# Performance work log

Measured on AMD Instinct MI355X. Metric: run time of the kernel, lower is better.

Reference implementation:

```python
import jax, jax.numpy as jnp
import numpy as np

N = 2048; C_IN = 2; H = 32; EMB = 16; OUT = 1; HORIZON = 12
B = 32; T = 16

def setup_inputs() -> dict:
    key = jax.random.key(0)
    ks = jax.random.split(key, 10)
    s = 0.05
    return {
        "x":  jax.random.normal(ks[0], (B, T, N, C_IN), dtype=jnp.float32),
        "E1": jax.random.normal(ks[1], (N, EMB), dtype=jnp.float32) * 0.1,
        "E2": jax.random.normal(ks[2], (N, EMB), dtype=jnp.float32) * 0.1,
        "Wx": jax.random.normal(ks[3], (C_IN, 4 * H), dtype=jnp.float32) * s,
        "bx": jnp.zeros((4 * H,), dtype=jnp.float32),
        "Wh": jax.random.normal(ks[4], (H, 4 * H), dtype=jnp.float32) * s,
        "bh": jnp.zeros((4 * H,), dtype=jnp.float32),
        "Wp": jax.random.normal(ks[5], (H, OUT * HORIZON), dtype=jnp.float32) * s,
        "bp": jnp.zeros((OUT * HORIZON,), dtype=jnp.float32),
    }

def reference(x, E1, E2, Wx, bx, Wh, bh, Wp, bp):
    Bb, Tt, Nn, _ = x.shape
    # adaptive adjacency: softmax(relu(E1 @ E2^T)) over last dim  [N,N]
    A = jax.nn.softmax(jax.nn.relu(E1 @ E2.T), axis=-1)

    def step(carry, xt):
        h, c = carry  # [B,N,H]
        # fused graph-conv gates: (A @ xt) Wx + (A @ h) Wh + biases -> [B,N,4H]
        gates = (jnp.einsum('ij,bjc->bic', A, xt) @ Wx + bx
                 + jnp.einsum('ij,bjh->bih', A, h) @ Wh + bh)
        i, f, o, g = jnp.split(gates, 4, axis=-1)
        i = jax.nn.sigmoid(i); f = jax.nn.sigmoid(f); o = jax.nn.sigmoid(o)
        g = jnp.tanh(g)
        c_t = f * c + i * g
        h_t = o * jnp.tanh(c_t)
        return (h_t, c_t), None

    h0 = jnp.zeros((Bb, Nn, H), dtype=x.dtype)
    c0 = jnp.zeros((Bb, Nn, H), dtype=x.dtype)
    (h_last, _), _ = jax.lax.scan(step, (h0, c0), jnp.transpose(x, (1, 0, 2, 3)))
    out = h_last @ Wp + bp                      # [B,N,horizon*out]
    out = out.reshape(Bb, Nn, HORIZON, OUT)
    return jnp.transpose(out, (0, 2, 1, 3))     # [B,horizon,N,out]
```

## Files before the change

### kernel.cpp

```cpp
#include <hip/hip_runtime.h>
#include <hip/hip_bf16.h>
#include <cstddef>
#include <cstdint>

#define NN 2048
#define CIN 2
#define HH 32
#define EMB 16
#define HOR 12
#define BB 32
#define TT 16
#define GC 128
#define XCOLS 1024
#define HCOLS 1024

#define ATILE_STRIDE 65536
#define BTILE_STRIDE 32768
#define LOPLANE 2097152

typedef __attribute__((ext_vector_type(8))) _Float16 f16x8;
typedef __attribute__((ext_vector_type(16))) float f32x16;

__device__ __forceinline__ void load_lds16(const void* g, void* l) {
    __builtin_amdgcn_global_load_lds(
        (const __attribute__((address_space(1))) void*)g,
        (__attribute__((address_space(3))) void*)l, 16, 0, 0);
}

__global__ __launch_bounds__(256) void precompute(const float* __restrict__ E1,
                                                  const float* __restrict__ E2,
                                                  const float* __restrict__ x,
                                                  const float* __restrict__ Wx,
                                                  const float* __restrict__ bx,
                                                  const float* __restrict__ Wh,
                                                  const float* __restrict__ bh,
                                                  _Float16* __restrict__ A2,
                                                  _Float16* __restrict__ B2x,
                                                  _Float16* __restrict__ W16,
                                                  float* __restrict__ Wxr,
                                                  float* __restrict__ bfold) {
    const int blk = blockIdx.x;
    const int tid = threadIdx.x;

    if (blk < NN) {
        const int i = blk;
        __shared__ float red[256];
        float e1[EMB];
#pragma unroll
        for (int k = 0; k < EMB; ++k) e1[k] = E1[i * EMB + k];

        float s[8];
        float mx = -1e30f;
#pragma unroll
        for (int q = 0; q < 8; ++q) {
            const int j = tid * 8 + q;
            float d = 0.f;
#pragma unroll
            for (int k = 0; k < EMB; ++k) d += e1[k] * E2[j * EMB + k];
            d = fmaxf(d, 0.0f);
            s[q] = d;
            mx = fmaxf(mx, d);
        }
        red[tid] = mx;
        __syncthreads();
        for (int off = 128; off > 0; off >>= 1) {
            if (tid < off) red[tid] = fmaxf(red[tid], red[tid + off]);
            __syncthreads();
        }
        mx = red[0];
        __syncthreads();

        float sum = 0.f;
#pragma unroll
        for (int q = 0; q < 8; ++q) { s[q] = expf(s[q] - mx); sum += s[q]; }
        red[tid] = sum;
        __syncthreads();
        for (int off = 128; off > 0; off >>= 1) {
            if (tid < off) red[tid] += red[tid + off];
            __syncthreads();
        }
        const float inv = 1.0f / red[0];
        f16x8 v;
#pragma unroll
        for (int q = 0; q < 8; ++q) v[q] = (_Float16)(s[q] * inv);
        *(f16x8*)(A2 + ((size_t)tid * 2048 + i) * 8) = v;
    } else if (blk < NN + 1024) {
        const int idx = (blk - NN) * 256 + tid;
        const int col = idx & 1023;
        const int jc  = idx >> 10;
        const int bt  = col >> 1;
        const int c   = col & 1;
        const float* xp = x + ((size_t)bt * NN + jc * 8) * CIN + c;
        f16x8 vh, vl;
#pragma unroll
        for (int e = 0; e < 8; ++e) {
            const float v = xp[e * CIN];
            const _Float16 hi = (_Float16)v;
            vh[e] = hi;
            vl[e] = (_Float16)(v - (float)hi);
        }
        const size_t base = ((size_t)jc * 1024 + col) * 8;
        *(f16x8*)(B2x + base) = vh;
        *(f16x8*)(B2x + base + LOPLANE) = vl;
    } else {
#pragma unroll
        for (int r = 0; r < 32; ++r) {
            const int idx = r * 256 + tid;
            const int e  = idx & 7;
            const int ln = (idx >> 3) & 63;
            const int gq = (idx >> 9) & 3;
            const int kh = (idx >> 11) & 1;
            const int k  = kh * 16 + (ln >> 5) * 8 + e;
            const int ch = gq * 32 + (ln & 31);
            const float v = Wh[k * GC + (ch & 3) * HH + (ch >> 2)];
            const _Float16 hi = (_Float16)v;
            W16[idx] = hi;
            W16[8192 + idx] = (_Float16)(v - (float)hi);
        }
        {
            const int idx = tid;
            const int c = idx >> 7, rem = idx & 127;
            const int h = rem >> 2, g = rem & 3;
            Wxr[idx] = Wx[c * GC + g * HH + h];
        }
        if (tid < 128) {
            const int h = tid >> 2, g = tid & 3;
            bfold[tid] = bx[g * HH + h] + bh[g * HH + h];
        }
    }
}

template <int NPROD, int GATE>
__global__ __launch_bounds__(512, 2) void gemm_fused(const _Float16* __restrict__ A2,
                                                     const _Float16* __restrict__ B2,
                                                     float* __restrict__ Cout,
                                                     const float* __restrict__ AX,
                                                     const _Float16* __restrict__ W16,
                                                     const float* __restrict__ Wxr,
                                                     const float* __restrict__ bfold,
                                                     float* __restrict__ cst,
                                                     float* __restrict__ h32,
                                                     _Float16* __restrict__ hTout,
                                                     int t, int last) {
    constexpr int SUBS   = (NPROD == 1) ? 2 : 1;
    constexpr int NT     = 64 / SUBS;
    constexpr int SUBBUF = 4096 + NPROD * 8192;
    constexpr int BUF    = SUBS * SUBBUF;
    constexpr int NBUF   = (NPROD == 1) ? 4 : 6;
    constexpr int PCH    = 256 + NPROD * 512;
    constexpr int NG     = (SUBS * PCH) / 64;
    constexpr int GMAX   = 3;
    constexpr int STAGE_SZ = NBUF * BUF;
    constexpr int SMEMSZ = GATE ? (STAGE_SZ + 1024 + 512 + 2048) : STAGE_SZ;
    __shared__ __align__(16) char smem[SMEMSZ];

    const int tid  = threadIdx.x;
    const int w    = tid >> 6;
    const int lane = tid & 63;

    const int wg = blockIdx.x;
    const int x8 = wg & 7;
    const int s  = wg >> 3;
    const int mb = (x8 >> 1) * 8 + (s & 7);
    const int nb = (x8 & 1) * 4 + (s >> 3);
    const int m0 = mb * 64;
    const int n0 = nb * 128;

    float* wxr_s = nullptr; float* bfl_s = nullptr; float* axs = nullptr;
    if constexpr (GATE) {
        wxr_s = (float*)(smem + STAGE_SZ);
        bfl_s = (float*)(smem + STAGE_SZ + 1024);
        axs   = (float*)(smem + STAGE_SZ + 1536);
        const int b0c = nb * 4;
        if (tid < 64) *(float4*)&wxr_s[tid * 4] = *(const float4*)&Wxr[tid * 4];
        if (tid < 32) *(float4*)&bfl_s[tid * 4] = *(const float4*)&bfold[tid * 4];
        axs[tid] = AX[(size_t)(m0 + (tid & 63)) * XCOLS +
                      ((b0c + (tid >> 7)) * TT + t) * CIN + ((tid >> 6) & 1)];
    }

    const _Float16* gp[GMAX];
    int lbase[GMAX];
    int adv[GMAX];
    bool val[GMAX];
#pragma unroll
    for (int i = 0; i < GMAX; ++i) {
        const int g = w + 8 * i;
        val[i] = (g < NG);
        const int gg = val[i] ? g : 0;
        const int cid  = gg * 64 + lane;
        const int cid0 = gg * 64;
        const int su  = cid / PCH,  r  = cid  - su * PCH;
        const int su0 = cid0 / PCH, r0 = cid0 - su0 * PCH;
        if (r < 256) {
            gp[i]  = A2 + ((size_t)((su * 4 + (r >> 6)) * 2048) + m0 + (r & 63)) * 8;
            adv[i] = SUBS * ATILE_STRIDE;
        } else {
            const int r2 = r - 256;
            gp[i]  = B2 + (size_t)(r2 >> 9) * LOPLANE
                        + ((size_t)((su * 4 + ((r2 & 511) >> 7)) * 1024) + n0 + (r2 & 127)) * 8;
            adv[i] = SUBS * BTILE_STRIDE;
        }
        lbase[i] = su0 * SUBBUF + (r0 < 256 ? r0 * 16 : 4096 + (r0 - 256) * 16);
    }

    const int lrow = lane & 31, lg = lane >> 5;
    const int mi = w >> 2;
    const int gq = w & 3;
    const int wc = gq * 32;
    const int aoff0 = lg * 1024 + (mi * 32 + lrow) * 16;
    const int aoff1 = 2048 + lg * 1024 + (mi * 32 + lrow) * 16;
    const int boff0 = 4096 + lg * 2048 + (wc + lrow) * 16;
    const int boff1 = 4096 + 4096 + lg * 2048 + (wc + lrow) * 16;

    f32x16 acc0 = (f32x16)(0.0f), acc1 = (f32x16)(0.0f);

#define STAGE(BUFI) do {                                                       \
    char* lb = smem + (BUFI) * BUF;                                            \
    _Pragma("unroll")                                                          \
    for (int i = 0; i < GMAX; ++i) if (val[i]) {                               \
        load_lds16(gp[i], lb + lbase[i]);                                      \
        gp[i] += adv[i];                                                       \
    }                                                                          \
} while (0)

#define VMW(NHI, NLO) do {                                                     \
    if (w < 4) asm volatile("s_waitcnt vmcnt(" #NHI ")" ::: "memory");         \
    else       asm volatile("s_waitcnt vmcnt(" #NLO ")" ::: "memory");         \
} while (0)

#define BAR() do {                                                             \
    __builtin_amdgcn_s_barrier();                                              \
    asm volatile("" ::: "memory");                                             \
} while (0)

#define COMPUTE(BUFI) do {                                                     \
    const char* sb = smem + (BUFI) * BUF;                                      \
    _Pragma("unroll")                                                          \
    for (int su = 0; su < SUBS; ++su) {                                        \
        const char* st = sb + su * SUBBUF;                                     \
        f16x8 fa0 = *(const f16x8*)(st + aoff0);                               \
        f16x8 fa1 = *(const f16x8*)(st + aoff1);                               \
        f16x8 fb0 = *(const f16x8*)(st + boff0);                               \
        f16x8 fb1 = *(const f16x8*)(st + boff1);                               \
        acc0 = __builtin_amdgcn_mfma_f32_32x32x16_f16(fa0, fb0, acc0, 0, 0, 0);\
        acc1 = __builtin_amdgcn_mfma_f32_32x32x16_f16(fa1, fb1, acc1, 0, 0, 0);\
        if constexpr (NPROD == 2) {                                            \
            f16x8 fc0 = *(const f16x8*)(st + boff0 + 8192);                    \
            f16x8 fc1 = *(const f16x8*)(st + boff1 + 8192);                    \
            acc0 = __builtin_amdgcn_mfma_f32_32x32x16_f16(fa0, fc0, acc0, 0, 0, 0); \
            acc1 = __builtin_amdgcn_mfma_f32_32x32x16_f16(fa1, fc1, acc1, 0, 0, 0); \
        }                                                                      \
    }                                                                          \
} while (0)

    if constexpr (NPROD == 1) {
        STAGE(0);
        STAGE(1);
#pragma unroll 1
        for (int it = 0; it < NT - 2; ++it) {
            STAGE((it + 2) & 3);
            asm volatile("s_waitcnt vmcnt(6)" ::: "memory");
            BAR();
            COMPUTE(it & 3);
        }
        asm volatile("s_waitcnt vmcnt(3)" ::: "memory");
        BAR();
        COMPUTE((NT - 2) & 3);
        asm volatile("s_waitcnt vmcnt(0)" ::: "memory");
        BAR();
        COMPUTE((NT - 1) & 3);
    } else {
        STAGE(0);
        STAGE(1);
        STAGE(2);
        int bs = 3, bc = 0;
#pragma unroll 1
        for (int it = 0; it < NT - 3; ++it) {
            STAGE(bs);
            VMW(9, 6);
            BAR();
            COMPUTE(bc);
            bs = (bs == 5) ? 0 : bs + 1;
            bc = (bc == 5) ? 0 : bc + 1;
        }
        VMW(6, 4);
        BAR();
        COMPUTE(bc); bc = (bc == 5) ? 0 : bc + 1;
        VMW(3, 2);
        BAR();
        COMPUTE(bc); bc = (bc == 5) ? 0 : bc + 1;
        asm volatile("s_waitcnt vmcnt(0)" ::: "memory");
        BAR();
        COMPUTE(bc);
    }
#undef STAGE
#undef VMW
#undef BAR
#undef COMPUTE

    if constexpr (!GATE) {
        const int colg = n0 + wc + lrow;
#pragma unroll
        for (int r = 0; r < 16; ++r) {
            const int rp = (r & 3) + 8 * (r >> 2) + 4 * lg;
            Cout[(size_t)(m0 + mi * 32 + rp) * XCOLS + colg] = acc0[r] + acc1[r];
        }
    } else {
        f16x8 wbh0 = *(const f16x8*)(W16 + ((size_t)(0 * 4 + gq) * 64 + lane) * 8);
        f16x8 wbh1 = *(const f16x8*)(W16 + ((size_t)(1 * 4 + gq) * 64 + lane) * 8);
        f16x8 wbl0 = *(const f16x8*)(W16 + 8192 + ((size_t)(0 * 4 + gq) * 64 + lane) * 8);
        f16x8 wbl1 = *(const f16x8*)(W16 + 8192 + ((size_t)(1 * 4 + gq) * 64 + lane) * 8);

        _Float16* ahh = (_Float16*)smem;
        _Float16* ahl = (_Float16*)(smem + 17408);
        const int colw = wc + lrow;
#pragma unroll
        for (int r = 0; r < 16; ++r) {
            const int rp = (r & 3) + 8 * (r >> 2) + 4 * lg;
            const float v = acc0[r] + acc1[r];
            const _Float16 hi = (_Float16)v;
            ahh[(mi * 32 + rp) * 136 + colw] = hi;
            ahl[(mi * 32 + rp) * 136 + colw] = (_Float16)(v - (float)hi);
        }
        __syncthreads();

        f32x16 g0 = (f32x16)(0.0f), g1 = (f32x16)(0.0f);
        f32x16 g2 = (f32x16)(0.0f), g3 = (f32x16)(0.0f);
#define GATEB(ACC, b) do {                                                         \
    const int arow = (mi * 32 + lrow) * 136 + (b) * 32 + lg * 8;                   \
    f16x8 fh0 = *(const f16x8*)(ahh + arow);                                       \
    f16x8 fl0 = *(const f16x8*)(ahl + arow);                                       \
    f16x8 fh1 = *(const f16x8*)(ahh + arow + 16);                                  \
    f16x8 fl1 = *(const f16x8*)(ahl + arow + 16);                                  \
    ACC = __builtin_amdgcn_mfma_f32_32x32x16_f16(fh0, wbh0, ACC, 0, 0, 0);         \
    ACC = __builtin_amdgcn_mfma_f32_32x32x16_f16(fh0, wbl0, ACC, 0, 0, 0);         \
    ACC = __builtin_amdgcn_mfma_f32_32x32x16_f16(fl0, wbh0, ACC, 0, 0, 0);         \
    ACC = __builtin_amdgcn_mfma_f32_32x32x16_f16(fh1, wbh1, ACC, 0, 0, 0);         \
    ACC = __builtin_amdgcn_mfma_f32_32x32x16_f16(fh1, wbl1, ACC, 0, 0, 0);         \
    ACC = __builtin_amdgcn_mfma_f32_32x32x16_f16(fl1, wbh1, ACC, 0, 0, 0);         \
} while (0)
        GATEB(g0, 0); GATEB(g1, 1); GATEB(g2, 2); GATEB(g3, 3);
#undef GATEB

        float* gl = (float*)(smem + 34816);
        const int nl2 = tid & 63;
        const int hb  = (tid >> 6) * 4;
        const int b0c = nb * 4;
        const int nd  = m0 + nl2;
        const size_t ntbase = ((size_t)((nd >> 5) * 4 + ((nd >> 3) & 3)) * 1024) * 8 + (nd & 7);

#define POINT(ACC, bi) do {                                                        \
    _Pragma("unroll")                                                              \
    for (int r = 0; r < 16; ++r) {                                                 \
        const int rp = (r & 3) + 8 * (r >> 2) + 4 * lg;                            \
        gl[(mi * 32 + rp) * 132 + gq * 32 + lrow] = ACC[r];                        \
    }                                                                              \
    __syncthreads();                                                               \
    {                                                                              \
        const float ax0 = axs[(bi) * 128 + nl2];                                   \
        const float ax1 = axs[(bi) * 128 + 64 + nl2];                              \
        const int bb = b0c + (bi);                                                 \
        const size_t off = (size_t)nd * HCOLS + bb * HH + hb;                      \
        const float4 co = *(const float4*)(cst + off);                             \
        const float cold[4] = {co.x, co.y, co.z, co.w};                            \
        float cn[4], hn[4];                                                        \
        _Pragma("unroll")                                                          \
        for (int p = 0; p < 4; ++p) {                                              \
            const int hh = hb + p;                                                 \
            const float4 gt = *(const float4*)(gl + nl2 * 132 + hh * 4);           \
            const float a0 = gt.x + bfl_s[hh*4+0] + ax0*wxr_s[hh*4+0] + ax1*wxr_s[128+hh*4+0]; \
            const float a1 = gt.y + bfl_s[hh*4+1] + ax0*wxr_s[hh*4+1] + ax1*wxr_s[128+hh*4+1]; \
            const float a2 = gt.z + bfl_s[hh*4+2] + ax0*wxr_s[hh*4+2] + ax1*wxr_s[128+hh*4+2]; \
            const float a3 = gt.w + bfl_s[hh*4+3] + ax0*wxr_s[hh*4+3] + ax1*wxr_s[128+hh*4+3]; \
            const float i_ = 1.0f / (1.0f + expf(-a0));                            \
            const float f_ = 1.0f / (1.0f + expf(-a1));                            \
            const float o_ = 1.0f / (1.0f + expf(-a2));                            \
            const float g_ = tanhf(a3);                                            \
            const float ct = f_ * cold[p] + i_ * g_;                               \
            cn[p] = ct;                                                            \
            hn[p] = o_ * tanhf(ct);                                                \
        }                                                                          \
        *(float4*)(cst + off) = make_float4(cn[0], cn[1], cn[2], cn[3]);           \
        if (last) *(float4*)(h32 + off) = make_float4(hn[0], hn[1], hn[2], hn[3]); \
        _Pragma("unroll")                                                          \
        for (int p = 0; p < 4; ++p)                                                \
            hTout[ntbase + (size_t)(bb * HH + hb + p) * 8] = (_Float16)hn[p];      \
    }                                                                              \
    __syncthreads();                                                               \
} while (0)
        POINT(g0, 0); POINT(g1, 1); POINT(g2, 2); POINT(g3, 3);
#undef POINT
    }
}

__global__ __launch_bounds__(256) void gate_update(const float* __restrict__ AX,
                                                   const float* __restrict__ Wxr,
                                                   const float* __restrict__ bfold,
                                                   float* __restrict__ c,
                                                   float* __restrict__ h32,
                                                   _Float16* __restrict__ hT) {
    const int n0 = blockIdx.x * 64;
    const int b0 = blockIdx.y * 4;
    const int tid = threadIdx.x;
    __shared__ float wxr[256];
    __shared__ float bfl[128];
    __shared__ float axs[2][64];

    if (tid < 64)  *(float4*)&wxr[tid * 4] = *(const float4*)&Wxr[tid * 4];
    if (tid < 32)  *(float4*)&bfl[tid * 4] = *(const float4*)&bfold[tid * 4];

    const int nl = tid & 63;
    const int hq = tid >> 6;

    const int nd = n0 + nl;
    const size_t ntbase = ((size_t)((nd >> 5) * 4 + ((nd >> 3) & 3)) * 1024) * 8 + (nd & 7);

#pragma unroll 1
    for (int bi = 0; bi < 4; ++bi) {
        const int b = b0 + bi;
        if (bi) __syncthreads();
        if (tid < 128) {
            const int which = tid >> 6, nls = tid & 63;
            axs[which][nls] = AX[(size_t)(n0 + nls) * XCOLS + (b * TT + 0) * CIN + which];
        }
        __syncthreads();

        const float ax0 = axs[0][nl], ax1 = axs[1][nl];
        float cn[8], hn[8];
#pragma unroll
        for (int u = 0; u < 8; ++u) {
            const int h = hq * 8 + u;
            float a0 = bfl[h * 4 + 0] + ax0 * wxr[h * 4 + 0] + ax1 * wxr[128 + h * 4 + 0];
            float a1 = bfl[h * 4 + 1] + ax0 * wxr[h * 4 + 1] + ax1 * wxr[128 + h * 4 + 1];
            float a2 = bfl[h * 4 + 2] + ax0 * wxr[h * 4 + 2] + ax1 * wxr[128 + h * 4 + 2];
            float a3 = bfl[h * 4 + 3] + ax0 * wxr[h * 4 + 3] + ax1 * wxr[128 + h * 4 + 3];
            const float i_ = 1.0f / (1.0f + expf(-a0));
            const float f_ = 1.0f / (1.0f + expf(-a1));
            const float o_ = 1.0f / (1.0f + expf(-a2));
            const float g_ = tanhf(a3);
            const float ct = i_ * g_;
            (void)f_;
            cn[u] = ct;
            hn[u] = o_ * tanhf(ct);
        }
        const size_t off = (size_t)nd * HCOLS + b * HH + hq * 8;
        *(float4*)(c + off)       = make_float4(cn[0], cn[1], cn[2], cn[3]);
        *(float4*)(c + off + 4)   = make_float4(cn[4], cn[5], cn[6], cn[7]);
        *(float4*)(h32 + off)     = make_float4(hn[0], hn[1], hn[2], hn[3]);
        *(float4*)(h32 + off + 4) = make_float4(hn[4], hn[5], hn[6], hn[7]);
#pragma unroll
        for (int u = 0; u < 8; ++u)
            hT[ntbase + (size_t)(b * HH + hq * 8 + u) * 8] = (_Float16)hn[u];
    }
}

__global__ __launch_bounds__(256) void head_kernel(const float* __restrict__ h,
                                                   const float* __restrict__ Wp,
                                                   const float* __restrict__ bp,
                                                   float* __restrict__ out) {
    const int idx = blockIdx.x * 256 + threadIdx.x;
    const int b = idx >> 11;
    const int n = idx & (NN - 1);
    float hv[HH];
    const float* hp = h + (size_t)n * HCOLS + b * HH;
#pragma unroll
    for (int k = 0; k < HH; ++k) hv[k] = hp[k];
#pragma unroll
    for (int th = 0; th < HOR; ++th) {
        float acc = bp[th];
#pragma unroll
        for (int k = 0; k < HH; ++k) acc += hv[k] * Wp[k * HOR + th];
        out[((size_t)b * HOR + th) * NN + n] = acc;
    }
}

extern "C" void kernel_launch(void* const* d_in, const int* in_sizes, int n_in,
                              void* d_out, int out_size, void* d_ws, size_t ws_size,
                              hipStream_t stream) {
    const float* x  = (const float*)d_in[0];
    const float* E1 = (const float*)d_in[1];
    const float* E2 = (const float*)d_in[2];
    const float* Wx = (const float*)d_in[3];
    const float* bx = (const float*)d_in[4];
    const float* Wh = (const float*)d_in[5];
    const float* bh = (const float*)d_in[6];
    const float* Wp = (const float*)d_in[7];
    const float* bp = (const float*)d_in[8];

    char* ws = (char*)d_ws;
    _Float16* A2  = (_Float16*)(ws);
    _Float16* B2x = (_Float16*)(ws + ( 8ull << 20));
    _Float16* hT0 = (_Float16*)(ws + (16ull << 20));
    _Float16* hT1 = (_Float16*)(ws + (20ull << 20));
    float* AX   = (float*)(ws + (24ull << 20));
    float* cst  = (float*)(ws + (32ull << 20));
    float* h32  = (float*)(ws + (40ull << 20));
    float* Wxr  = (float*)(ws + (48ull << 20) + 65536);
    float* bfold= (float*)(ws + (48ull << 20) + 131072);
    _Float16* W16 = (_Float16*)(ws + (48ull << 20) + 262144);
    _Float16* hTb[2] = {hT0, hT1};

    precompute<<<NN + 1024 + 1, 256, 0, stream>>>(E1, E2, x, Wx, bx, Wh, bh,
                                                  A2, B2x, W16, Wxr, bfold);

    gemm_fused<2, 0><<<256, 512, 0, stream>>>(A2, B2x, AX, nullptr, nullptr, nullptr,
                                              nullptr, nullptr, nullptr, nullptr, 0, 0);

    gate_update<<<dim3(NN / 64, BB / 4), 256, 0, stream>>>(AX, Wxr, bfold,
                                                           cst, h32, hTb[0]);
    for (int t = 1; t < TT; ++t) {
        gemm_fused<1, 1><<<256, 512, 0, stream>>>(A2, hTb[(t + 1) & 1], nullptr, AX,
                                                  W16, Wxr, bfold, cst, h32,
                                                  hTb[t & 1], t, t == TT - 1 ? 1 : 0);
    }

    head_kernel<<<(BB * NN) / 256, 256, 0, stream>>>(h32, Wp, bp, (float*)d_out);
}
```

Baseline: 546.0 us.

## Transpose E2 and compute adjacency softmax one row per wavefront with shuffles

Adds a small kernel that transposes E2 so the adjacency-row computation reads it with coalesced loads. Each wavefront now handles a full row of 2048 columns, 32 per lane, and reduces max and sum with wave shuffles instead of block-wide shared-memory reductions and syncthreads. The A2 store becomes scattered 2-byte writes rather than 16-byte vector stores. This adds one extra kernel launch and more register pressure from the 32-element array.

```diff
diff --git a/kernel.cpp b/kernel.cpp
--- a/kernel.cpp
+++ b/kernel.cpp
@@ -27,8 +27,16 @@
         (__attribute__((address_space(3))) void*)l, 16, 0, 0);
 }
 
+__global__ __launch_bounds__(256) void e2_transpose(const float* __restrict__ E2,
+                                                    float* __restrict__ E2T) {
+    const int idx = blockIdx.x * 256 + threadIdx.x;
+    const int k = idx >> 11;
+    const int j = idx & 2047;
+    E2T[idx] = E2[j * EMB + k];
+}
+
 __global__ __launch_bounds__(256) void precompute(const float* __restrict__ E1,
-                                                  const float* __restrict__ E2,
+                                                  const float* __restrict__ E2T,
                                                   const float* __restrict__ x,
                                                   const float* __restrict__ Wx,
                                                   const float* __restrict__ bx,
@@ -42,50 +50,41 @@
     const int blk = blockIdx.x;
     const int tid = threadIdx.x;
 
-    if (blk < NN) {
-        const int i = blk;
-        __shared__ float red[256];
+    if (blk < 512) {
+        const int i = blk * 4 + (tid >> 6);
+        const int l = tid & 63;
         float e1[EMB];
 #pragma unroll
         for (int k = 0; k < EMB; ++k) e1[k] = E1[i * EMB + k];
 
-        float s[8];
-        float mx = -1e30f;
-#pragma unroll
-        for (int q = 0; q < 8; ++q) {
-            const int j = tid * 8 + q;
-            float d = 0.f;
-#pragma unroll
-            for (int k = 0; k < EMB; ++k) d += e1[k] * E2[j * EMB + k];
-            d = fmaxf(d, 0.0f);
-            s[q] = d;
-            mx = fmaxf(mx, d);
-        }
-        red[tid] = mx;
-        __syncthreads();
-        for (int off = 128; off > 0; off >>= 1) {
-            if (tid < off) red[tid] = fmaxf(red[tid], red[tid + off]);
-            __syncthreads();
-        }
-        mx = red[0];
-        __syncthreads();
-
+        float s[32];
+#pragma unroll
+        for (int c = 0; c < 32; ++c) s[c] = 0.f;
+#pragma unroll
+        for (int k = 0; k < EMB; ++k) {
+            const float ek = e1[k];
+            const float* p = E2T + k * 2048 + l;
+#pragma unroll
+            for (int c = 0; c < 32; ++c) s[c] = fmaf(ek, p[c * 64], s[c]);
+        }
+        float mx = 0.f;
+#pragma unroll
+        for (int c = 0; c < 32; ++c) { s[c] = fmaxf(s[c], 0.f); mx = fmaxf(mx, s[c]); }
+#pragma unroll
+        for (int off = 32; off > 0; off >>= 1) mx = fmaxf(mx, __shfl_xor(mx, off, 64));
         float sum = 0.f;
 #pragma unroll
-        for (int q = 0; q < 8; ++q) { s[q] = expf(s[q] - mx); sum += s[q]; }
-        red[tid] = sum;
-        __syncthreads();
-        for (int off = 128; off > 0; off >>= 1) {
-            if (tid < off) red[tid] += red[tid + off];
-            __syncthreads();
-        }
-        const float inv = 1.0f / red[0];
-        f16x8 v;
-#pragma unroll
-        for (int q = 0; q < 8; ++q) v[q] = (_Float16)(s[q] * inv);
-        *(f16x8*)(A2 + ((size_t)tid * 2048 + i) * 8) = v;
-    } else if (blk < NN + 1024) {
-        const int idx = (blk - NN) * 256 + tid;
+        for (int c = 0; c < 32; ++c) { s[c] = expf(s[c] - mx); sum += s[c]; }
+#pragma unroll
+        for (int off = 32; off > 0; off >>= 1) sum += __shfl_xor(sum, off, 64);
+        const float inv = 1.0f / sum;
+        const int chb = (l >> 3);
+        const int e   = l & 7;
+#pragma unroll
+        for (int c = 0; c < 32; ++c)
+            A2[((size_t)(c * 8 + chb) * 2048 + i) * 8 + e] = (_Float16)(s[c] * inv);
+    } else if (blk < 512 + 1024) {
+        const int idx = (blk - 512) * 256 + tid;
         const int col = idx & 1023;
         const int jc  = idx >> 10;
         const int bt  = col >> 1;
@@ -498,10 +497,13 @@
     float* Wxr  = (float*)(ws + (48ull << 20) + 65536);
     float* bfold= (float*)(ws + (48ull << 20) + 131072);
     _Float16* W16 = (_Float16*)(ws + (48ull << 20) + 262144);
+    float* E2T  = (float*)(ws + (48ull << 20) + 524288);
     _Float16* hTb[2] = {hT0, hT1};
 
-    precompute<<<NN + 1024 + 1, 256, 0, stream>>>(E1, E2, x, Wx, bx, Wh, bh,
-                                                  A2, B2x, W16, Wxr, bfold);
+    e2_transpose<<<128, 256, 0, stream>>>(E2, E2T);
+
+    precompute<<<512 + 1024 + 1, 256, 0, stream>>>(E1, E2T, x, Wx, bx, Wh, bh,
+                                                   A2, B2x, W16, Wxr, bfold);
 
     gemm_fused<2, 0><<<256, 512, 0, stream>>>(A2, B2x, AX, nullptr, nullptr, nullptr,
                                               nullptr, nullptr, nullptr, nullptr, 0, 0);
```

Measured after the change: 531.1 us. 2.7% less time.
